# Kernel optimization log

Hardware: AMD Instinct MI355X
Metric: run time of the kernel (lower is better)

## Reference

```python
import jax, jax.numpy as jnp
import numpy as np

D = 1024
H = 16
DH = D // H


def setup_inputs() -> dict:
    key = jax.random.key(0)
    ks = jax.random.split(key, 12)
    s = 0.02
    return {
        "x": jax.random.normal(ks[0], (2, 2048, D), dtype=jnp.float32),
        "ln1_g": jnp.ones((D,), jnp.float32),
        "ln1_b": jnp.zeros((D,), jnp.float32),
        "W_attn": jax.random.normal(ks[1], (3 * D, D), jnp.float32) * s,
        "b_attn": jnp.zeros((3 * D,), jnp.float32),
        "W_proj": jax.random.normal(ks[2], (D, D), jnp.float32) * s,
        "b_proj": jnp.zeros((D,), jnp.float32),
        "ln2_g": jnp.ones((D,), jnp.float32),
        "ln2_b": jnp.zeros((D,), jnp.float32),
        "W_up": jax.random.normal(ks[3], (4 * D, D), jnp.float32) * s,
        "b_up": jnp.zeros((4 * D,), jnp.float32),
        "W_down": jax.random.normal(ks[4], (D, 4 * D), jnp.float32) * s,
        "b_down": jnp.zeros((D,), jnp.float32),
    }


def layernorm(x, g, b, eps=1e-5):
    mu = jnp.mean(x, axis=-1, keepdims=True)
    var = jnp.mean(jnp.square(x - mu), axis=-1, keepdims=True)
    return (x - mu) * jax.lax.rsqrt(var + eps) * g + b


def new_gelu(x):
    c = np.sqrt(2.0 / np.pi).astype(np.float32)
    return 0.5 * x * (1.0 + jnp.tanh(c * (x + 0.044715 * x ** 3)))


def reference(x, ln1_g, ln1_b, W_attn, b_attn, W_proj, b_proj, ln2_g, ln2_b, W_up, b_up, W_down, b_down):
    b, s, d = x.shape
    h = layernorm(x, ln1_g, ln1_b)
    qkv = h @ W_attn.T + b_attn  # [b,s,3d]
    q, k, v = jnp.split(qkv, 3, axis=-1)
    # [b, H, s, DH]
    q = q.reshape(b, s, H, DH).transpose(0, 2, 1, 3)
    k = k.reshape(b, s, H, DH).transpose(0, 2, 1, 3)
    v = v.reshape(b, s, H, DH).transpose(0, 2, 1, 3)
    scores = jnp.einsum("bhqd,bhkd->bhqk", q, k) / np.sqrt(DH).astype(np.float32)
    causal = jnp.tril(jnp.ones((s, s), dtype=bool))
    scores = jnp.where(causal, scores, -jnp.inf)
    attn = jax.nn.softmax(scores, axis=-1)
    o = jnp.einsum("bhqk,bhkd->bhqd", attn, v).transpose(0, 2, 1, 3).reshape(b, s, d)
    x = x + o @ W_proj.T + b_proj
    h2 = layernorm(x, ln2_g, ln2_b)
    mlp = new_gelu(h2 @ W_up.T + b_up) @ W_down.T + b_down
    return x + mlp
```

## Files before the change

### kernel.cpp

```cpp
#include <hip/hip_runtime.h>
#include <hip/hip_bf16.h>

typedef __hip_bfloat16 bf16;
using bf16x8 = __attribute__((ext_vector_type(8))) short;
using bf16x4 = __attribute__((ext_vector_type(4))) short;
using f32x4  = __attribute__((ext_vector_type(4))) float;

#define D_MODEL 1024
#define SEQ     2048
#define NTOK    4096
#define NHEAD   16
#define DHEAD   64

__device__ inline f32x4 mfma16(bf16x8 a, bf16x8 b, f32x4 c) {
  return __builtin_amdgcn_mfma_f32_16x16x32_bf16(a, b, c, 0, 0, 0);
}

__device__ inline f32x4 mfma16k16(bf16x4 a, bf16x4 b, f32x4 c) {
#if __has_builtin(__builtin_amdgcn_mfma_f32_16x16x16bf16_1k)
  return __builtin_amdgcn_mfma_f32_16x16x16bf16_1k(a, b, c, 0, 0, 0);
#else
  f32x4 d;
  asm("v_mfma_f32_16x16x16_bf16 %0, %1, %2, %3" : "=v"(d) : "v"(a), "v"(b), "v"(c));
  return d;
#endif
}

__device__ inline void glds16(const void* g, void* l) {
  __builtin_amdgcn_global_load_lds(
      (const __attribute__((address_space(1))) unsigned int*)g,
      (__attribute__((address_space(3))) unsigned int*)l, 16, 0, 0);
}

__global__ __launch_bounds__(256) void f2bf_kernel(const float* __restrict__ in,
                                                   bf16* __restrict__ out, int n) {
  int i = (blockIdx.x * 256 + threadIdx.x) * 4;
  if (i >= n) return;
  float4 v = *(const float4*)(in + i);
  out[i + 0] = __float2bfloat16(v.x);
  out[i + 1] = __float2bfloat16(v.y);
  out[i + 2] = __float2bfloat16(v.z);
  out[i + 3] = __float2bfloat16(v.w);
}

__global__ __launch_bounds__(256) void ln_kernel(const float* __restrict__ x,
                                                 const float* __restrict__ g,
                                                 const float* __restrict__ bta,
                                                 bf16* __restrict__ out) {
  int row = blockIdx.x;
  int tid = threadIdx.x;
  const float* xr = x + (size_t)row * D_MODEL;
  float4 v = *(const float4*)(xr + tid * 4);
  float s  = v.x + v.y + v.z + v.w;
  float s2 = v.x * v.x + v.y * v.y + v.z * v.z + v.w * v.w;
  for (int o = 32; o > 0; o >>= 1) {
    s  += __shfl_down(s, o);
    s2 += __shfl_down(s2, o);
  }
  __shared__ float red[8];
  int wave = tid >> 6, lane = tid & 63;
  if (lane == 0) { red[wave] = s; red[4 + wave] = s2; }
  __syncthreads();
  s  = red[0] + red[1] + red[2] + red[3];
  s2 = red[4] + red[5] + red[6] + red[7];
  float mu  = s * (1.f / D_MODEL);
  float var = s2 * (1.f / D_MODEL) - mu * mu;
  float rs  = rsqrtf(var + 1e-5f);
  float4 gv = *(const float4*)(g + tid * 4);
  float4 bv = *(const float4*)(bta + tid * 4);
  bf16* orow = out + (size_t)row * D_MODEL + tid * 4;
  orow[0] = __float2bfloat16((v.x - mu) * rs * gv.x + bv.x);
  orow[1] = __float2bfloat16((v.y - mu) * rs * gv.y + bv.y);
  orow[2] = __float2bfloat16((v.z - mu) * rs * gv.z + bv.z);
  orow[3] = __float2bfloat16((v.w - mu) * rs * gv.w + bv.w);
}

#define EP_BIAS_BF16      0
#define EP_BIAS_GELU_BF16 1
#define EP_BIAS_RES_F32   2

template <int EP>
__device__ inline void ep_store(void* out, const float* res, size_t off, float v) {
  if (EP == EP_BIAS_BF16) {
    ((bf16*)out)[off] = __float2bfloat16(v);
  } else if (EP == EP_BIAS_GELU_BF16) {
    float u = 0.7978845608f * (v + 0.044715f * v * v * v);
    float gl = v / (1.0f + __expf(-2.0f * u));
    ((bf16*)out)[off] = __float2bfloat16(gl);
  } else {
    ((float*)out)[off] = res[off] + v;
  }
}

template <int EP>
__global__ __launch_bounds__(256, 2) void gemm_nt(const bf16* __restrict__ A,
                                                  const bf16* __restrict__ W,
                                                  const float* __restrict__ bias,
                                                  const float* res, void* out,
                                                  int M, int N, int K) {
  __shared__ short sA[128 * 64];
  __shared__ short sB[128 * 64];
  int tid  = threadIdx.x;
  int wave = tid >> 6, lane = tid & 63;
  int quad = lane >> 4, l16 = lane & 15;
  int wm = (wave >> 1) * 64, wn = (wave & 1) * 64;
  int bm = blockIdx.x * 128, bn = blockIdx.y * 128;

  int rl = lane >> 3;
  int cz = (lane & 7) ^ rl;
  const bf16* aptr[4];
  const bf16* bptr[4];
#pragma unroll
  for (int i = 0; i < 4; i++) {
    int j = wave * 4 + i;
    aptr[i] = A + (size_t)(bm + j * 8 + rl) * K + cz * 8;
    bptr[i] = W + (size_t)(bn + j * 8 + rl) * K + cz * 8;
  }

  f32x4 acc[4][4] = {};

  for (int k0 = 0; k0 < K; k0 += 64) {
    __syncthreads();
#pragma unroll
    for (int i = 0; i < 4; i++) {
      glds16(aptr[i] + k0, (char*)sA + (wave * 4 + i) * 1024);
      glds16(bptr[i] + k0, (char*)sB + (wave * 4 + i) * 1024);
    }
    __builtin_amdgcn_s_waitcnt(0);
    __syncthreads();

#pragma unroll
    for (int kk = 0; kk < 2; kk++) {
      int cq = kk * 4 + quad;
      int sw = (cq ^ (l16 & 7)) * 8;
      bf16x8 af[4], bfr[4];
#pragma unroll
      for (int t = 0; t < 4; t++) {
        af[t]  = *(const bf16x8*)&sA[(wm + t * 16 + l16) * 64 + sw];
        bfr[t] = *(const bf16x8*)&sB[(wn + t * 16 + l16) * 64 + sw];
      }
#pragma unroll
      for (int mt = 0; mt < 4; mt++)
#pragma unroll
        for (int nt = 0; nt < 4; nt++)
          acc[mt][nt] = mfma16(af[mt], bfr[nt], acc[mt][nt]);
    }
  }

#pragma unroll
  for (int mt = 0; mt < 4; mt++)
#pragma unroll
    for (int nt = 0; nt < 4; nt++) {
      int col = bn + wn + nt * 16 + l16;
      float bs = bias[col];
#pragma unroll
      for (int i = 0; i < 4; i++) {
        int row = bm + wm + mt * 16 + quad * 4 + i;
        ep_store<EP>(out, res, (size_t)row * N + col, acc[mt][nt][i] + bs);
      }
    }
}

template <int EP>
__global__ __launch_bounds__(256, 2) void gemm_nt2(const bf16* __restrict__ A,
                                                   const bf16* __restrict__ W,
                                                   const float* __restrict__ bias,
                                                   const float* res, void* out,
                                                   int M, int N, int K) {
  __shared__ short sA[128 * 64];
  __shared__ short sB[64 * 64];
  int tid  = threadIdx.x;
  int wave = tid >> 6, lane = tid & 63;
  int quad = lane >> 4, l16 = lane & 15;
  int wm = wave * 32;
  int bm = blockIdx.x * 128, bn = blockIdx.y * 64;

  int rl = lane >> 3;
  int cz = (lane & 7) ^ rl;
  const bf16* aptr[4];
  const bf16* bptr[2];
#pragma unroll
  for (int i = 0; i < 4; i++)
    aptr[i] = A + (size_t)(bm + (wave * 4 + i) * 8 + rl) * K + cz * 8;
#pragma unroll
  for (int i = 0; i < 2; i++)
    bptr[i] = W + (size_t)(bn + (wave * 2 + i) * 8 + rl) * K + cz * 8;

  f32x4 acc[2][4] = {};

  for (int k0 = 0; k0 < K; k0 += 64) {
    __syncthreads();
#pragma unroll
    for (int i = 0; i < 4; i++)
      glds16(aptr[i] + k0, (char*)sA + (wave * 4 + i) * 1024);
#pragma unroll
    for (int i = 0; i < 2; i++)
      glds16(bptr[i] + k0, (char*)sB + (wave * 2 + i) * 1024);
    __builtin_amdgcn_s_waitcnt(0);
    __syncthreads();

#pragma unroll
    for (int kk = 0; kk < 2; kk++) {
      int cq = kk * 4 + quad;
      int sw = (cq ^ (l16 & 7)) * 8;
      bf16x8 af[2], bfr[4];
#pragma unroll
      for (int t = 0; t < 2; t++)
        af[t] = *(const bf16x8*)&sA[(wm + t * 16 + l16) * 64 + sw];
#pragma unroll
      for (int t = 0; t < 4; t++)
        bfr[t] = *(const bf16x8*)&sB[(t * 16 + l16) * 64 + sw];
#pragma unroll
      for (int mt = 0; mt < 2; mt++)
#pragma unroll
        for (int nt = 0; nt < 4; nt++)
          acc[mt][nt] = mfma16(af[mt], bfr[nt], acc[mt][nt]);
    }
  }

#pragma unroll
  for (int mt = 0; mt < 2; mt++)
#pragma unroll
    for (int nt = 0; nt < 4; nt++) {
      int col = bn + nt * 16 + l16;
      float bs = bias[col];
#pragma unroll
      for (int i = 0; i < 4; i++) {
        int row = bm + wm + mt * 16 + quad * 4 + i;
        ep_store<EP>(out, res, (size_t)row * N + col, acc[mt][nt][i] + bs);
      }
    }
}

__global__ __launch_bounds__(256, 2) void attn_kernel(const short* __restrict__ qkvS,
                                                      short* __restrict__ oS) {
  int bh = blockIdx.y;
  int b = bh >> 4, h = bh & 15;
  int tid = threadIdx.x, wave = tid >> 6, lane = tid & 63;
  int quad = lane >> 4, l16 = lane & 15;
  const int RS = 3 * D_MODEL;
  const short* base = qkvS + (size_t)b * SEQ * RS;
  const int koff = D_MODEL + h * 64, voff = 2 * D_MODEL + h * 64, qoff = h * 64;
  const float c2 = 0.1803368801f;

  __shared__ short sK[64 * 64];
  __shared__ short sV[64 * 64];

  int rl = lane >> 3;
  int cz = (lane & 7) ^ rl;
  int vkr = tid >> 3, vd0 = (tid & 7) * 8;

  auto run_pass = [&](int q0p) {
    int qrow = q0p + wave * 16 + l16;
    bf16x8 qf0 = *(const bf16x8*)&base[(size_t)qrow * RS + qoff + quad * 8];
    bf16x8 qf1 = *(const bf16x8*)&base[(size_t)qrow * RS + qoff + 32 + quad * 8];

    f32x4 oacc[4] = {};
    float lsum = 0.f;
    int ntile = q0p / 64 + 1;

    bf16x8 vreg0, vreg1;
    {
      const short* vp = &base[(size_t)vkr * RS + voff + vd0];
      vreg0 = *(const bf16x8*)vp;
      vreg1 = *(const bf16x8*)(vp + (size_t)32 * RS);
    }

    for (int t = 0; t < ntile; t++) {
      int kv0 = t * 64;
      __syncthreads();

#pragma unroll
      for (int i = 0; i < 2; i++) {
        int j = wave * 2 + i;
        glds16(&base[(size_t)(kv0 + j * 8 + rl) * RS + koff + cz * 8],
               (char*)sK + j * 1024);
      }
      __asm__ __volatile__("" ::: "memory");

      bf16x8 nv0, nv1;
      bool more = (t + 1 < ntile);
      if (more) {
        const short* vp = &base[(size_t)((t + 1) * 64 + vkr) * RS + voff + vd0];
        nv0 = *(const bf16x8*)vp;
        nv1 = *(const bf16x8*)(vp + (size_t)32 * RS);
      }

      {
        int kvl = vkr, c4 = kvl >> 2;
#pragma unroll
        for (int j = 0; j < 8; j++)
          sV[c4 * 256 + ((vd0 + j + c4) & 63) * 4 + (kvl & 3)] = vreg0[j];
        kvl = vkr + 32; c4 = kvl >> 2;
#pragma unroll
        for (int j = 0; j < 8; j++)
          sV[c4 * 256 + ((vd0 + j + c4) & 63) * 4 + (kvl & 3)] = vreg1[j];
      }

      __asm__ __volatile__("" ::: "memory");
      if (more) __builtin_amdgcn_s_waitcnt(0x0002);
      else      __builtin_amdgcn_s_waitcnt(0x0000);
      __builtin_amdgcn_s_barrier();
      __asm__ __volatile__("" ::: "memory");

      f32x4 st[4];
#pragma unroll
      for (int t16 = 0; t16 < 4; t16++) {
        bf16x8 kf0 = *(const bf16x8*)&sK[(t16 * 16 + l16) * 64 + ((quad ^ (l16 & 7)) * 8)];
        bf16x8 kf1 = *(const bf16x8*)&sK[(t16 * 16 + l16) * 64 + (((quad + 4) ^ (l16 & 7)) * 8)];
        f32x4 z = {};
        z = mfma16(kf0, qf0, z);
        st[t16] = mfma16(kf1, qf1, z);
      }

      bool diag = (t == ntile - 1);
      int qg = q0p + wave * 16 + l16;
#pragma unroll
      for (int t16 = 0; t16 < 4; t16++) {
        bf16x4 pf;
        int kvb = kv0 + t16 * 16 + quad * 4;
#pragma unroll
        for (int i = 0; i < 4; i++) {
          float p = exp2f(fminf(st[t16][i] * c2, 30.f));
          if (diag && (kvb + i > qg)) p = 0.f;
          lsum += p;
          pf[i] = __builtin_bit_cast(short, __float2bfloat16(p));
        }
        int c4 = t16 * 4 + quad;
#pragma unroll
        for (int dt = 0; dt < 4; dt++) {
          bf16x4 vb = *(const bf16x4*)&sV[c4 * 256 + ((dt * 16 + l16 + c4) & 63) * 4];
          oacc[dt] = mfma16k16(pf, vb, oacc[dt]);
        }
      }

      if (more) { vreg0 = nv0; vreg1 = nv1; }
    }

    lsum += __shfl_xor(lsum, 16);
    lsum += __shfl_xor(lsum, 32);
    float inv[4];
#pragma unroll
    for (int i = 0; i < 4; i++) inv[i] = 1.0f / __shfl(lsum, quad * 4 + i);
#pragma unroll
    for (int dt = 0; dt < 4; dt++)
#pragma unroll
      for (int i = 0; i < 4; i++) {
        int row = q0p + wave * 16 + quad * 4 + i;
        int col = qoff + dt * 16 + l16;
        oS[((size_t)b * SEQ + row) * D_MODEL + col] =
            __builtin_bit_cast(short, __float2bfloat16(oacc[dt][i] * inv[i]));
      }
  };

  run_pass(blockIdx.x * 64);
  run_pass((31 - blockIdx.x) * 64);
}

extern "C" void kernel_launch(void* const* d_in, const int* in_sizes, int n_in,
                              void* d_out, int out_size, void* d_ws, size_t ws_size,
                              hipStream_t stream) {
  const float* x      = (const float*)d_in[0];
  const float* ln1_g  = (const float*)d_in[1];
  const float* ln1_b  = (const float*)d_in[2];
  const float* W_attn = (const float*)d_in[3];
  const float* b_attn = (const float*)d_in[4];
  const float* W_proj = (const float*)d_in[5];
  const float* b_proj = (const float*)d_in[6];
  const float* ln2_g  = (const float*)d_in[7];
  const float* ln2_b  = (const float*)d_in[8];
  const float* W_up   = (const float*)d_in[9];
  const float* b_up   = (const float*)d_in[10];
  const float* W_down = (const float*)d_in[11];
  const float* b_down = (const float*)d_in[12];
  float* out = (float*)d_out;

  char* p = (char*)d_ws;
  bf16* Wattn_b = (bf16*)p; p += (size_t)3 * D_MODEL * D_MODEL * 2;
  bf16* Wproj_b = (bf16*)p; p += (size_t)D_MODEL * D_MODEL * 2;
  bf16* Wup_b   = (bf16*)p; p += (size_t)4 * D_MODEL * D_MODEL * 2;
  bf16* Wdown_b = (bf16*)p; p += (size_t)4 * D_MODEL * D_MODEL * 2;
  bf16* h_b     = (bf16*)p; p += (size_t)NTOK * D_MODEL * 2;
  bf16* qkv_b   = (bf16*)p; p += (size_t)NTOK * 3 * D_MODEL * 2;
  bf16* o_b     = (bf16*)p; p += (size_t)NTOK * D_MODEL * 2;
  bf16* h2_b    = (bf16*)p; p += (size_t)NTOK * D_MODEL * 2;
  bf16* up_b    = (bf16*)p; p += (size_t)NTOK * 4 * D_MODEL * 2;

  {
    int n1 = 3 * D_MODEL * D_MODEL, n2 = D_MODEL * D_MODEL, n3 = 4 * D_MODEL * D_MODEL;
    f2bf_kernel<<<n1 / 1024, 256, 0, stream>>>(W_attn, Wattn_b, n1);
    f2bf_kernel<<<n2 / 1024, 256, 0, stream>>>(W_proj, Wproj_b, n2);
    f2bf_kernel<<<n3 / 1024, 256, 0, stream>>>(W_up, Wup_b, n3);
    f2bf_kernel<<<n3 / 1024, 256, 0, stream>>>(W_down, Wdown_b, n3);
  }
  ln_kernel<<<NTOK, 256, 0, stream>>>(x, ln1_g, ln1_b, h_b);
  gemm_nt<EP_BIAS_BF16><<<dim3(NTOK / 128, 3 * D_MODEL / 128), 256, 0, stream>>>(
      h_b, Wattn_b, b_attn, nullptr, qkv_b, NTOK, 3 * D_MODEL, D_MODEL);
  attn_kernel<<<dim3(16, 2 * NHEAD), 256, 0, stream>>>((const short*)qkv_b, (short*)o_b);
  gemm_nt2<EP_BIAS_RES_F32><<<dim3(NTOK / 128, D_MODEL / 64), 256, 0, stream>>>(
      o_b, Wproj_b, b_proj, x, out, NTOK, D_MODEL, D_MODEL);
  ln_kernel<<<NTOK, 256, 0, stream>>>(out, ln2_g, ln2_b, h2_b);
  gemm_nt<EP_BIAS_GELU_BF16><<<dim3(NTOK / 128, 4 * D_MODEL / 128), 256, 0, stream>>>(
      h2_b, Wup_b, b_up, nullptr, up_b, NTOK, 4 * D_MODEL, D_MODEL);
  gemm_nt2<EP_BIAS_RES_F32><<<dim3(NTOK / 128, D_MODEL / 64), 256, 0, stream>>>(
      up_b, Wdown_b, b_down, out, out, NTOK, D_MODEL, 4 * D_MODEL);
}
```

Baseline: 359.9 us.

## Merge attention query passes over shared KV tiles, fuse weight casts, raise GEMM occupancy

The attention kernel now handles both of its query blocks in a single sweep over the KV tiles, so each K/V tile is loaded into shared memory once and used by both blocks instead of being reloaded in two passes. The V shared-memory layout switches to an XOR swizzle and the output stores use a permuted column mapping. The four weight-cast launches become one kernel, and both GEMM kernels raise the launch-bounds occupancy hint from 2 to 3. The occupancy hint may force register spills, and holding both query blocks' accumulators at once raises register pressure in the attention kernel.

Result: faster. 341.8 us (-5.0%).

```diff
diff --git a/kernel.cpp b/kernel.cpp
--- a/kernel.cpp
+++ b/kernel.cpp
@@ -32,15 +32,23 @@
       (__attribute__((address_space(3))) unsigned int*)l, 16, 0, 0);
 }
 
-__global__ __launch_bounds__(256) void f2bf_kernel(const float* __restrict__ in,
-                                                   bf16* __restrict__ out, int n) {
-  int i = (blockIdx.x * 256 + threadIdx.x) * 4;
-  if (i >= n) return;
-  float4 v = *(const float4*)(in + i);
-  out[i + 0] = __float2bfloat16(v.x);
-  out[i + 1] = __float2bfloat16(v.y);
-  out[i + 2] = __float2bfloat16(v.z);
-  out[i + 3] = __float2bfloat16(v.w);
+__global__ __launch_bounds__(256) void f2bf4_kernel(const float* __restrict__ s0,
+                                                    const float* __restrict__ s1,
+                                                    const float* __restrict__ s2,
+                                                    const float* __restrict__ s3,
+                                                    bf16* __restrict__ dst) {
+  const size_t M1 = (size_t)D_MODEL * D_MODEL;
+  size_t i = ((size_t)blockIdx.x * 256 + threadIdx.x) * 4;
+  const float* s; size_t off;
+  if (i < 3 * M1)      { s = s0; off = i; }
+  else if (i < 4 * M1) { s = s1; off = i - 3 * M1; }
+  else if (i < 8 * M1) { s = s2; off = i - 4 * M1; }
+  else                 { s = s3; off = i - 8 * M1; }
+  float4 v = *(const float4*)(s + off);
+  dst[i + 0] = __float2bfloat16(v.x);
+  dst[i + 1] = __float2bfloat16(v.y);
+  dst[i + 2] = __float2bfloat16(v.z);
+  dst[i + 3] = __float2bfloat16(v.w);
 }
 
 __global__ __launch_bounds__(256) void ln_kernel(const float* __restrict__ x,
@@ -93,7 +101,7 @@
 }
 
 template <int EP>
-__global__ __launch_bounds__(256, 2) void gemm_nt(const bf16* __restrict__ A,
+__global__ __launch_bounds__(256, 3) void gemm_nt(const bf16* __restrict__ A,
                                                   const bf16* __restrict__ W,
                                                   const float* __restrict__ bias,
                                                   const float* res, void* out,
@@ -162,7 +170,7 @@
 }
 
 template <int EP>
-__global__ __launch_bounds__(256, 2) void gemm_nt2(const bf16* __restrict__ A,
+__global__ __launch_bounds__(256, 3) void gemm_nt2(const bf16* __restrict__ A,
                                                    const bf16* __restrict__ W,
                                                    const float* __restrict__ bias,
                                                    const float* res, void* out,
@@ -236,6 +244,8 @@
                                                       short* __restrict__ oS) {
   int bh = blockIdx.y;
   int b = bh >> 4, h = bh & 15;
+  int iq = blockIdx.x;
+  int qa = iq * 64, qb = (31 - iq) * 64;
   int tid = threadIdx.x, wave = tid >> 6, lane = tid & 63;
   int quad = lane >> 4, l16 = lane & 15;
   const int RS = 3 * D_MODEL;
@@ -246,115 +256,117 @@
   __shared__ short sK[64 * 64];
   __shared__ short sV[64 * 64];
 
-  int rl = lane >> 3;
-  int cz = (lane & 7) ^ rl;
+  int rl = lane >> 3, cz = (lane & 7) ^ rl;
   int vkr = tid >> 3, vd0 = (tid & 7) * 8;
-
-  auto run_pass = [&](int q0p) {
-    int qrow = q0p + wave * 16 + l16;
-    bf16x8 qf0 = *(const bf16x8*)&base[(size_t)qrow * RS + qoff + quad * 8];
-    bf16x8 qf1 = *(const bf16x8*)&base[(size_t)qrow * RS + qoff + 32 + quad * 8];
-
-    f32x4 oacc[4] = {};
-    float lsum = 0.f;
-    int ntile = q0p / 64 + 1;
-
-    bf16x8 vreg0, vreg1;
-    {
-      const short* vp = &base[(size_t)vkr * RS + voff + vd0];
-      vreg0 = *(const bf16x8*)vp;
-      vreg1 = *(const bf16x8*)(vp + (size_t)32 * RS);
-    }
-
-    for (int t = 0; t < ntile; t++) {
-      int kv0 = t * 64;
-      __syncthreads();
-
-#pragma unroll
-      for (int i = 0; i < 2; i++) {
-        int j = wave * 2 + i;
-        glds16(&base[(size_t)(kv0 + j * 8 + rl) * RS + koff + cz * 8],
-               (char*)sK + j * 1024);
-      }
-      __asm__ __volatile__("" ::: "memory");
-
-      bf16x8 nv0, nv1;
-      bool more = (t + 1 < ntile);
-      if (more) {
-        const short* vp = &base[(size_t)((t + 1) * 64 + vkr) * RS + voff + vd0];
-        nv0 = *(const bf16x8*)vp;
-        nv1 = *(const bf16x8*)(vp + (size_t)32 * RS);
-      }
-
-      {
-        int kvl = vkr, c4 = kvl >> 2;
-#pragma unroll
-        for (int j = 0; j < 8; j++)
-          sV[c4 * 256 + ((vd0 + j + c4) & 63) * 4 + (kvl & 3)] = vreg0[j];
-        kvl = vkr + 32; c4 = kvl >> 2;
-#pragma unroll
-        for (int j = 0; j < 8; j++)
-          sV[c4 * 256 + ((vd0 + j + c4) & 63) * 4 + (kvl & 3)] = vreg1[j];
-      }
-
-      __asm__ __volatile__("" ::: "memory");
-      if (more) __builtin_amdgcn_s_waitcnt(0x0002);
-      else      __builtin_amdgcn_s_waitcnt(0x0000);
-      __builtin_amdgcn_s_barrier();
-      __asm__ __volatile__("" ::: "memory");
-
+  int vb7 = tid & 7;
+  int kv3 = vkr & 3;
+  int c4lo = vkr >> 2, c4hi = c4lo + 8;
+  int xpar = (c4lo & 1) << 3;
+
+  int qrA = qa + wave * 16 + l16, qrB = qb + wave * 16 + l16;
+  bf16x8 qA0 = *(const bf16x8*)&base[(size_t)qrA * RS + qoff + quad * 8];
+  bf16x8 qA1 = *(const bf16x8*)&base[(size_t)qrA * RS + qoff + 32 + quad * 8];
+  bf16x8 qB0 = *(const bf16x8*)&base[(size_t)qrB * RS + qoff + quad * 8];
+  bf16x8 qB1 = *(const bf16x8*)&base[(size_t)qrB * RS + qoff + 32 + quad * 8];
+
+  f32x4 oA[4] = {}, oB[4] = {};
+  float lsA = 0.f, lsB = 0.f;
+  int ntile = 32 - iq;
+
+  bf16x8 v0, v1;
+  {
+    const short* vp = &base[(size_t)vkr * RS + voff + vd0];
+    v0 = *(const bf16x8*)vp;
+    v1 = *(const bf16x8*)(vp + (size_t)32 * RS);
+  }
+
+  for (int t = 0; t < ntile; t++) {
+    int kv0 = t * 64;
+    __syncthreads();
+#pragma unroll
+    for (int ii = 0; ii < 2; ii++) {
+      int j = wave * 2 + ii;
+      glds16(&base[(size_t)(kv0 + j * 8 + rl) * RS + koff + cz * 8], (char*)sK + j * 1024);
+    }
+    __asm__ __volatile__("" ::: "memory");
+
+    bf16x8 nv0, nv1;
+    bool more = (t + 1 < ntile);
+    if (more) {
+      const short* vp = &base[(size_t)((t + 1) * 64 + vkr) * RS + voff + vd0];
+      nv0 = *(const bf16x8*)vp;
+      nv1 = *(const bf16x8*)(vp + (size_t)32 * RS);
+    }
+
+#pragma unroll
+    for (int j = 0; j < 8; j++)
+      sV[c4lo * 256 + (vb7 | ((j << 3) ^ xpar)) * 4 + kv3] = v0[j];
+#pragma unroll
+    for (int j = 0; j < 8; j++)
+      sV[c4hi * 256 + (vb7 | ((j << 3) ^ xpar)) * 4 + kv3] = v1[j];
+
+    __asm__ __volatile__("" ::: "memory");
+    if (more) __builtin_amdgcn_s_waitcnt(0x0002);
+    else      __builtin_amdgcn_s_waitcnt(0x0000);
+    __builtin_amdgcn_s_barrier();
+    __asm__ __volatile__("" ::: "memory");
+
+    auto do_q = [&](bf16x8 q0, bf16x8 q1, f32x4* oo, float& ls, bool diag, int qg) {
       f32x4 st[4];
 #pragma unroll
       for (int t16 = 0; t16 < 4; t16++) {
         bf16x8 kf0 = *(const bf16x8*)&sK[(t16 * 16 + l16) * 64 + ((quad ^ (l16 & 7)) * 8)];
         bf16x8 kf1 = *(const bf16x8*)&sK[(t16 * 16 + l16) * 64 + (((quad + 4) ^ (l16 & 7)) * 8)];
         f32x4 z = {};
-        z = mfma16(kf0, qf0, z);
-        st[t16] = mfma16(kf1, qf1, z);
-      }
-
-      bool diag = (t == ntile - 1);
-      int qg = q0p + wave * 16 + l16;
+        z = mfma16(kf0, q0, z);
+        st[t16] = mfma16(kf1, q1, z);
+      }
 #pragma unroll
       for (int t16 = 0; t16 < 4; t16++) {
         bf16x4 pf;
         int kvb = kv0 + t16 * 16 + quad * 4;
 #pragma unroll
-        for (int i = 0; i < 4; i++) {
-          float p = exp2f(fminf(st[t16][i] * c2, 30.f));
-          if (diag && (kvb + i > qg)) p = 0.f;
-          lsum += p;
-          pf[i] = __builtin_bit_cast(short, __float2bfloat16(p));
+        for (int e = 0; e < 4; e++) {
+          float p = exp2f(fminf(st[t16][e] * c2, 30.f));
+          if (diag && (kvb + e > qg)) p = 0.f;
+          ls += p;
+          pf[e] = __builtin_bit_cast(short, __float2bfloat16(p));
         }
-        int c4 = t16 * 4 + quad;
+        int c4r = t16 * 4 + quad;
+        int xr = (c4r & 1) << 3;
 #pragma unroll
         for (int dt = 0; dt < 4; dt++) {
-          bf16x4 vb = *(const bf16x4*)&sV[c4 * 256 + ((dt * 16 + l16 + c4) & 63) * 4];
-          oacc[dt] = mfma16k16(pf, vb, oacc[dt]);
+          int pr = (dt * 16 + l16) ^ xr;
+          bf16x4 vb = *(const bf16x4*)&sV[c4r * 256 + pr * 4];
+          oo[dt] = mfma16k16(pf, vb, oo[dt]);
         }
       }
-
-      if (more) { vreg0 = nv0; vreg1 = nv1; }
-    }
-
-    lsum += __shfl_xor(lsum, 16);
-    lsum += __shfl_xor(lsum, 32);
+    };
+
+    do_q(qB0, qB1, oB, lsB, t == ntile - 1, qb + wave * 16 + l16);
+    if (t <= iq) do_q(qA0, qA1, oA, lsA, t == iq, qa + wave * 16 + l16);
+
+    if (more) { v0 = nv0; v1 = nv1; }
+  }
+
+  auto finish = [&](f32x4* oo, float ls, int q0p) {
+    ls += __shfl_xor(ls, 16);
+    ls += __shfl_xor(ls, 32);
     float inv[4];
 #pragma unroll
-    for (int i = 0; i < 4; i++) inv[i] = 1.0f / __shfl(lsum, quad * 4 + i);
+    for (int e = 0; e < 4; e++) inv[e] = 1.0f / __shfl(ls, quad * 4 + e);
+    int sigbase = ((l16 & 7) << 3) | (l16 >> 3);
 #pragma unroll
     for (int dt = 0; dt < 4; dt++)
 #pragma unroll
-      for (int i = 0; i < 4; i++) {
-        int row = q0p + wave * 16 + quad * 4 + i;
-        int col = qoff + dt * 16 + l16;
-        oS[((size_t)b * SEQ + row) * D_MODEL + col] =
-            __builtin_bit_cast(short, __float2bfloat16(oacc[dt][i] * inv[i]));
+      for (int e = 0; e < 4; e++) {
+        int row = q0p + wave * 16 + quad * 4 + e;
+        oS[((size_t)b * SEQ + row) * D_MODEL + qoff + sigbase + dt * 2] =
+            __builtin_bit_cast(short, __float2bfloat16(oo[dt][e] * inv[e]));
       }
   };
-
-  run_pass(blockIdx.x * 64);
-  run_pass((31 - blockIdx.x) * 64);
+  finish(oB, lsB, qb);
+  finish(oA, lsA, qa);
 }
 
 extern "C" void kernel_launch(void* const* d_in, const int* in_sizes, int n_in,
@@ -387,11 +399,8 @@
   bf16* up_b    = (bf16*)p; p += (size_t)NTOK * 4 * D_MODEL * 2;
 
   {
-    int n1 = 3 * D_MODEL * D_MODEL, n2 = D_MODEL * D_MODEL, n3 = 4 * D_MODEL * D_MODEL;
-    f2bf_kernel<<<n1 / 1024, 256, 0, stream>>>(W_attn, Wattn_b, n1);
-    f2bf_kernel<<<n2 / 1024, 256, 0, stream>>>(W_proj, Wproj_b, n2);
-    f2bf_kernel<<<n3 / 1024, 256, 0, stream>>>(W_up, Wup_b, n3);
-    f2bf_kernel<<<n3 / 1024, 256, 0, stream>>>(W_down, Wdown_b, n3);
+    size_t ntot = (size_t)12 * D_MODEL * D_MODEL;
+    f2bf4_kernel<<<(int)(ntot / 1024), 256, 0, stream>>>(W_attn, W_proj, W_up, W_down, Wattn_b);
   }
   ln_kernel<<<NTOK, 256, 0, stream>>>(x, ln1_g, ln1_b, h_b);
   gemm_nt<EP_BIAS_BF16><<<dim3(NTOK / 128, 3 * D_MODEL / 128), 256, 0, stream>>>(
```
